# Optimization experiments

Measured on AMD Instinct MI355X. Metric: run time of the kernel, lower is better.

## Reference

```python
import jax, jax.numpy as jnp
import numpy as np

B, S, D, H = 2, 2048, 1024, 16
HW = D // H  # head width = 64
MASK_FILL = -100000000.0


def setup_inputs() -> dict:
    key0 = jax.random.key(0)
    ks = jax.random.split(key0, 12)
    inp = {
        "query": jax.random.normal(ks[0], (B, S, D), jnp.float32),
        "key": jax.random.normal(ks[1], (B, S, D), jnp.float32),
        "value": jax.random.normal(ks[2], (B, S, D), jnp.float32),
        # bool mask, True masks; broadcasts over batch and heads
        "mask": jax.random.randint(ks[3], (S, S), 0, 2).astype(jnp.bool_),
        # per-head projection kernels: (heads, head_width, d_in)
        "Wq": jax.random.normal(ks[4], (H, HW, D), jnp.float32) * 0.02,
        "bq": jnp.zeros((H, HW), jnp.float32),
        "Wk": jax.random.normal(ks[5], (H, HW, D), jnp.float32) * 0.02,
        "bk": jnp.zeros((H, HW), jnp.float32),
        "Wv": jax.random.normal(ks[6], (H, HW, D), jnp.float32) * 0.02,
        "bv": jnp.zeros((H, HW), jnp.float32),
        # collapse projector: contracts (heads, head_width) -> d_output
        "Wo": jax.random.normal(ks[7], (D, H, HW), jnp.float32) * 0.02,
        "bo": jnp.zeros((D,), jnp.float32),
    }
    return inp


def reference(query, key, value, mask, Wq, bq, Wk, bk, Wv, bv, Wo, bo):
    # head projections -> (b, h, s, w)
    q = jnp.einsum("bsd,hwd->bhsw", query, Wq) + bq[:, None, :]
    k = jnp.einsum("btd,hwd->bhtw", key, Wk) + bk[:, None, :]
    v = jnp.einsum("btd,hwd->bhtw", value, Wv) + bv[:, None, :]
    # unscaled logits, masked_fill, softmax (matches original exactly)
    logits = jnp.einsum("bhsw,bhtw->bhst", q, k)
    logits = jnp.where(mask, MASK_FILL, logits)
    score = jax.nn.softmax(logits, axis=-1)
    # NOTE: original divides AV output by sqrt(head_width) AFTER softmax
    attn = jnp.einsum("bhst,bhtw->bhsw", score, v) / jnp.sqrt(jnp.float32(HW))
    # collapse heads -> (b, s, d_output)
    out = jnp.einsum("bhsw,ohw->bso", attn, Wo) + bo
    return out
```

## Files before the change

kernel.cpp:

```cpp
#include <hip/hip_runtime.h>
#include <hip/hip_bf16.h>
#include <math.h>

#define S_LEN   2048
#define D_MODEL 1024
#define N_HEADS 16
#define HEAD_W  64
#define BATCH   2
#define MROWS   (BATCH * S_LEN)
#define MASK_FILL -100000000.0f
#define LOG2E 1.4426950408889634f

typedef __attribute__((ext_vector_type(8))) short bf16x8;
typedef __attribute__((ext_vector_type(4))) float f32x4;
typedef unsigned short u16;
typedef unsigned int   u32;
typedef unsigned long long u64;

__device__ __forceinline__ u16 f2bf(float f) {
    u32 u = __float_as_uint(f);
    return (u16)((u + 0x7fffu + ((u >> 16) & 1u)) >> 16);
}

__device__ __forceinline__ u32 pack_bf16x2(float lo, float hi) {
    __hip_bfloat162 t = __float22bfloat162_rn(make_float2(lo, hi));
    u32 r;
    __builtin_memcpy(&r, &t, 4);
    return r;
}

__device__ __forceinline__ void gld_lds16(const void* gp, void* lp) {
    __builtin_amdgcn_global_load_lds(
        (const __attribute__((address_space(1))) u32*)gp,
        (__attribute__((address_space(3))) u32*)lp, 16, 0, 0);
}

struct CvtJobs {
    const float* src[7];
    u16* dst[7];
    int n[7];
};
__global__ __launch_bounds__(256) void prep_kernel(
    CvtJobs j, const unsigned char* __restrict__ mask, u64* __restrict__ bits) {
    const int t = blockIdx.y;
    if (t < 7) {
        const float* s = j.src[t];
        u16* d = j.dst[t];
        const int n = j.n[t];
        int i = (blockIdx.x * 256 + threadIdx.x) * 4;
        if (i < n) {
            float4 v = *(const float4*)(s + i);
            ushort4 o;
            o.x = f2bf(v.x); o.y = f2bf(v.y); o.z = f2bf(v.z); o.w = f2bf(v.w);
            *(ushort4*)(d + i) = o;
        }
        return;
    }
    if (blockIdx.x >= 2048) return;
    __shared__ int isByte;
    if (threadIdx.x == 0) isByte = 0;
    __syncthreads();
    const int e0 = blockIdx.x * 2048;
    const uint2 v = ((const uint2*)(mask + e0))[threadIdx.x];
    if (((v.x | v.y) & 0xFFFFFF00u) != 0u) isByte = 1;
    __syncthreads();
    const int ib = isByte;
    const int* mi = (const int*)mask;
#pragma unroll
    for (int jj = 0; jj < 8; ++jj) {
        const int e = e0 + jj * 256 + threadIdx.x;
        const bool m = ib ? (mask[e] != 0) : (mi[e] != 0);
        const u64 bl = __ballot(m);
        if ((e & 63) == 0) bits[e >> 6] = bl;
    }
}

__device__ __forceinline__ void gemm_core_64(const u16* __restrict__ A,
                                             const u16* __restrict__ Bt,
                                             int m0, int n0, f32x4 acc[2][4]) {
    __shared__ u16 As[2][2048];
    __shared__ u16 Bs[2][4096];
    const int tid = threadIdx.x;
    const int wv = tid >> 6, ln = tid & 63;
    const int lane16 = ln & 15, quad = ln >> 4;
    const int wr = (wv >> 1) * 32, wc = (wv & 1) * 64;
    const u16* Ap = A + (size_t)(m0 + ln) * D_MODEL + wv * 8;
    const u16* B0 = Bt + (size_t)(n0 + ln) * D_MODEL + wv * 8;
    const u16* B1 = Bt + (size_t)(n0 + 64 + ln) * D_MODEL + wv * 8;

    gld_lds16(Ap, &As[0][wv * 512]);
    gld_lds16(B0, &Bs[0][wv * 1024]);
    gld_lds16(B1, &Bs[0][wv * 1024 + 512]);

    for (int kt = 0; kt < D_MODEL / 32; ++kt) {
        const int buf = kt & 1;
        __syncthreads();
        if (kt < D_MODEL / 32 - 1) {
            const int ko = (kt + 1) * 32;
            gld_lds16(Ap + ko, &As[buf ^ 1][wv * 512]);
            gld_lds16(B0 + ko, &Bs[buf ^ 1][wv * 1024]);
            gld_lds16(B1 + ko, &Bs[buf ^ 1][wv * 1024 + 512]);
        }
        bf16x8 af[2], bfv[4];
#pragma unroll
        for (int mt = 0; mt < 2; ++mt)
            af[mt] = *(const bf16x8*)&As[buf][quad * 512 + (wr + mt * 16 + lane16) * 8];
#pragma unroll
        for (int nt = 0; nt < 4; ++nt)
            bfv[nt] = *(const bf16x8*)&Bs[buf][quad * 1024 + (wc + nt * 16 + lane16) * 8];
#pragma unroll
        for (int mt = 0; mt < 2; ++mt)
#pragma unroll
            for (int nt = 0; nt < 4; ++nt)
                acc[mt][nt] = __builtin_amdgcn_mfma_f32_16x16x32_bf16(
                    af[mt], bfv[nt], acc[mt][nt], 0, 0, 0);
    }
}

__global__ __launch_bounds__(256, 4) void qkv_gemm_kernel(
    const u16* __restrict__ xq, const u16* __restrict__ xk, const u16* __restrict__ xv,
    const u16* __restrict__ wq, const u16* __restrict__ wk, const u16* __restrict__ wv,
    const float* __restrict__ bq, const float* __restrict__ bk, const float* __restrict__ bv,
    u16* __restrict__ qb, u16* __restrict__ kb, u16* __restrict__ vbt) {
    const int z = blockIdx.z;
    const int tid = threadIdx.x;
    const int wvi = tid >> 6, ln = tid & 63;
    const int lane16 = ln & 15, quad = ln >> 4;
    const int wr = (wvi >> 1) * 32, wc = (wvi & 1) * 64;
    f32x4 acc[2][4] = {};

    if (z == 2) {
        const int m0 = (blockIdx.y & 15) * 64;
        const int n0 = (((blockIdx.y >> 4) * 8) + blockIdx.x) * 128;
        gemm_core_64(wv, xv, m0, n0, acc);
#pragma unroll
        for (int mt = 0; mt < 2; ++mt)
#pragma unroll
            for (int r = 0; r < 4; ++r) {
                const int m = m0 + wr + mt * 16 + quad * 4 + r;
                const int h = m >> 6, w = m & 63;
                const float bb = bv[m];
#pragma unroll
                for (int nt = 0; nt < 4; ++nt) {
                    const int n = n0 + wc + nt * 16 + lane16;
                    const int bidx = n >> 11, t = n & 2047;
                    vbt[((size_t)((bidx * N_HEADS + h) * HEAD_W + w)) * S_LEN + t] =
                        f2bf(acc[mt][nt][r] + bb);
                }
            }
        return;
    }

    const u16* A = (z == 0) ? xq : xk;
    const u16* Bt = (z == 0) ? wq : wk;
    const float* bias = (z == 0) ? bq : bk;
    u16* outp = (z == 0) ? qb : kb;
    const float scale = (z == 0) ? LOG2E : 1.0f;
    const int m0 = blockIdx.y * 64, n0 = blockIdx.x * 128;
    gemm_core_64(A, Bt, m0, n0, acc);
#pragma unroll
    for (int nt = 0; nt < 4; ++nt) {
        const int n = n0 + wc + nt * 16 + lane16;
        const float bb = bias[n];
        const int h = n >> 6, w = n & 63;
#pragma unroll
        for (int mt = 0; mt < 2; ++mt)
#pragma unroll
            for (int r = 0; r < 4; ++r) {
                const int m = m0 + wr + mt * 16 + quad * 4 + r;
                const int bidx = m >> 11, s = m & 2047;
                outp[((size_t)((bidx * N_HEADS + h) * S_LEN + s)) * HEAD_W + w] =
                    f2bf((acc[mt][nt][r] + bb) * scale);
            }
    }
}

__global__ __launch_bounds__(256, 4) void out_gemm_kernel(
    const u16* __restrict__ ab, const u16* __restrict__ wo,
    const float* __restrict__ bo, float* __restrict__ out) {
    f32x4 acc[2][4] = {};
    const int m0 = blockIdx.y * 64, n0 = blockIdx.x * 128;
    gemm_core_64(ab, wo, m0, n0, acc);
    const int tid = threadIdx.x;
    const int wvi = tid >> 6, ln = tid & 63;
    const int lane16 = ln & 15, quad = ln >> 4;
    const int wr = (wvi >> 1) * 32, wc = (wvi & 1) * 64;
#pragma unroll
    for (int nt = 0; nt < 4; ++nt) {
        const int n = n0 + wc + nt * 16 + lane16;
        const float bb = bo[n];
#pragma unroll
        for (int mt = 0; mt < 2; ++mt)
#pragma unroll
            for (int r = 0; r < 4; ++r) {
                const int m = m0 + wr + mt * 16 + quad * 4 + r;
                out[(size_t)m * D_MODEL + n] = acc[mt][nt][r] + bb;
            }
    }
}

__global__ __launch_bounds__(256, 3) void attn_kernel(
    const u16* __restrict__ qbuf, const u16* __restrict__ kbuf,
    const u16* __restrict__ vbt, const u64* __restrict__ mbits,
    float* __restrict__ Opart, float* __restrict__ lpart) {
    __shared__ u16 Ks[2][4096];
    __shared__ u16 Vt[2][4096];
    __shared__ u16 Ps[4][32 * 72];
    const int tid = threadIdx.x;
    const int wv = tid >> 6, ln = tid & 63;
    const int lane16 = ln & 15, quad = ln >> 4;
    const int s_blk = blockIdx.x * 128;
    const int h = blockIdx.y;
    const int b = blockIdx.z >> 1, hf = blockIdx.z & 1;
    const int c0 = hf * 16;
    const size_t hb = ((size_t)(b * N_HEADS + h)) * S_LEN * HEAD_W;
    const u16* Qg = qbuf + hb;
    const u16* Kg = kbuf + hb;
    const u16* Vg = vbt + hb;

    bf16x8 qa[2][2];
#pragma unroll
    for (int mt = 0; mt < 2; ++mt)
#pragma unroll
        for (int kk = 0; kk < 2; ++kk)
            qa[mt][kk] = *(const bf16x8*)(Qg +
                (size_t)(s_blk + wv * 32 + mt * 16 + lane16) * HEAD_W + kk * 32 + quad * 8);

    const size_t mrow0 = (size_t)(s_blk + wv * 32 + lane16) * 32;
    const size_t mrow1 = (size_t)(s_blk + wv * 32 + 16 + lane16) * 32;
    u64 mwCur0 = mbits[mrow0 + c0], mwCur1 = mbits[mrow1 + c0];
    u64 mwNx0 = 0, mwNx1 = 0;

    {
        const int t0g = c0 * 64;
        const int i0 = 2 * wv, i1 = 2 * wv + 1;
        gld_lds16(Kg + (size_t)(t0g + ln) * HEAD_W + i0 * 8, &Ks[0][i0 * 512]);
        gld_lds16(Kg + (size_t)(t0g + ln) * HEAD_W + i1 * 8, &Ks[0][i1 * 512]);
        gld_lds16(Vg + (size_t)ln * S_LEN + t0g + i0 * 8, &Vt[0][i0 * 512]);
        gld_lds16(Vg + (size_t)ln * S_LEN + t0g + i1 * 8, &Vt[0][i1 * 512]);
    }

    f32x4 oacc[2][4] = {};
    float lsum[2] = {0.0f, 0.0f};

    for (int ci = 0; ci < 16; ++ci) {
        const int c = c0 + ci;
        const int buf = ci & 1;
        __syncthreads();
        if (ci < 15) {
            const int t1 = (c + 1) * 64;
            const int i0 = 2 * wv, i1 = 2 * wv + 1;
            gld_lds16(Kg + (size_t)(t1 + ln) * HEAD_W + i0 * 8, &Ks[buf ^ 1][i0 * 512]);
            gld_lds16(Kg + (size_t)(t1 + ln) * HEAD_W + i1 * 8, &Ks[buf ^ 1][i1 * 512]);
            gld_lds16(Vg + (size_t)ln * S_LEN + t1 + i0 * 8, &Vt[buf ^ 1][i0 * 512]);
            gld_lds16(Vg + (size_t)ln * S_LEN + t1 + i1 * 8, &Vt[buf ^ 1][i1 * 512]);
            mwNx0 = mbits[mrow0 + c + 1];
            mwNx1 = mbits[mrow1 + c + 1];
        }

        f32x4 st[4][2] = {};
#pragma unroll
        for (int kk = 0; kk < 2; ++kk)
#pragma unroll
            for (int ntT = 0; ntT < 4; ++ntT) {
                bf16x8 kf = *(const bf16x8*)&Ks[buf][(kk * 4 + quad) * 512 + (ntT * 16 + lane16) * 8];
#pragma unroll
                for (int mt = 0; mt < 2; ++mt)
                    st[ntT][mt] = __builtin_amdgcn_mfma_f32_16x16x32_bf16(
                        kf, qa[mt][kk], st[ntT][mt], 0, 0, 0);
            }

#pragma unroll
        for (int mt = 0; mt < 2; ++mt) {
            const u64 mw = mt ? mwCur1 : mwCur0;
            float ls0 = 0.0f, ls1 = 0.0f;
#pragma unroll
            for (int ntT = 0; ntT < 4; ++ntT) {
                const u32 nib = (u32)(mw >> (ntT * 16 + quad * 4)) & 15u;
                float p0 = exp2f(st[ntT][mt][0]); if (nib & 1u) p0 = 0.0f;
                float p1 = exp2f(st[ntT][mt][1]); if (nib & 2u) p1 = 0.0f;
                float p2 = exp2f(st[ntT][mt][2]); if (nib & 4u) p2 = 0.0f;
                float p3 = exp2f(st[ntT][mt][3]); if (nib & 8u) p3 = 0.0f;
                ls0 += p0 + p1;
                ls1 += p2 + p3;
                uint2 pk;
                pk.x = pack_bf16x2(p0, p1);
                pk.y = pack_bf16x2(p2, p3);
                *(uint2*)&Ps[wv][(mt * 16 + lane16) * 72 + ntT * 16 + quad * 4] = pk;
            }
            lsum[mt] += ls0 + ls1;
        }

        bf16x8 pf[2][2];
#pragma unroll
        for (int mt = 0; mt < 2; ++mt)
#pragma unroll
            for (int kk = 0; kk < 2; ++kk)
                pf[mt][kk] = *(const bf16x8*)&Ps[wv][(mt * 16 + lane16) * 72 + kk * 32 + quad * 8];
#pragma unroll
        for (int kk = 0; kk < 2; ++kk)
#pragma unroll
            for (int ntw = 0; ntw < 4; ++ntw) {
                bf16x8 vf = *(const bf16x8*)&Vt[buf][(kk * 4 + quad) * 512 + (ntw * 16 + lane16) * 8];
#pragma unroll
                for (int mt = 0; mt < 2; ++mt)
                    oacc[mt][ntw] = __builtin_amdgcn_mfma_f32_16x16x32_bf16(
                        pf[mt][kk], vf, oacc[mt][ntw], 0, 0, 0);
            }
        mwCur0 = mwNx0; mwCur1 = mwNx1;
    }

    float* OpB = Opart + ((size_t)(hf * 4096 + b * 2048)) * 1024;
#pragma unroll
    for (int mt = 0; mt < 2; ++mt) {
#pragma unroll
        for (int r = 0; r < 4; ++r) {
            const int s = s_blk + wv * 32 + mt * 16 + quad * 4 + r;
            float* dst = OpB + (size_t)s * 1024 + h * 64;
#pragma unroll
            for (int ntw = 0; ntw < 4; ++ntw)
                dst[ntw * 16 + lane16] = oacc[mt][ntw][r];
        }
        float lm = lsum[mt];
        lm += __shfl_xor(lm, 16);
        lm += __shfl_xor(lm, 32);
        if (quad == 0) {
            const int srow = s_blk + wv * 32 + mt * 16 + lane16;
            lpart[(size_t)(hf * 4096 + b * 2048 + srow) * 16 + h] = lm;
        }
    }
}

__global__ __launch_bounds__(256) void combine_kernel(
    const float* __restrict__ Op, const float* __restrict__ lp,
    u16* __restrict__ ab) {
    const int idx4 = blockIdx.x * 256 + threadIdx.x;
    const int row = idx4 >> 8;
    const int d = (idx4 & 255) * 4;
    const int h = d >> 6;
    const float l = lp[(size_t)row * 16 + h] + lp[(size_t)(4096 + row) * 16 + h];
    const float inv = 0.125f / l;
    float4 a = *(const float4*)(Op + (size_t)row * 1024 + d);
    float4 b = *(const float4*)(Op + (size_t)(4096 + row) * 1024 + d);
    ushort4 o;
    o.x = f2bf((a.x + b.x) * inv);
    o.y = f2bf((a.y + b.y) * inv);
    o.z = f2bf((a.z + b.z) * inv);
    o.w = f2bf((a.w + b.w) * inv);
    *(ushort4*)(ab + (size_t)row * 1024 + d) = o;
}

extern "C" void kernel_launch(void* const* d_in, const int* in_sizes, int n_in,
                              void* d_out, int out_size, void* d_ws, size_t ws_size,
                              hipStream_t stream) {
    const float* query = (const float*)d_in[0];
    const float* key   = (const float*)d_in[1];
    const float* value = (const float*)d_in[2];
    const void*  mask  = d_in[3];
    const float* Wq = (const float*)d_in[4];
    const float* bq = (const float*)d_in[5];
    const float* Wk = (const float*)d_in[6];
    const float* bk = (const float*)d_in[7];
    const float* Wv = (const float*)d_in[8];
    const float* bv = (const float*)d_in[9];
    const float* Wo = (const float*)d_in[10];
    const float* bo = (const float*)d_in[11];
    float* out = (float*)d_out;

    char* ws = (char*)d_ws;
    const size_t MB = 1024 * 1024;
    u64* bits = (u64*)ws;
    u16* wob  = (u16*)(ws + 1 * MB);
    u16* qb   = (u16*)(ws + 3 * MB);
    u16* kb   = (u16*)(ws + 11 * MB);
    u16* vbt  = (u16*)(ws + 19 * MB);
    char* uA = ws + 27 * MB;
    u16* xq   = (u16*)(uA);
    u16* xk   = (u16*)(uA + 8 * MB);
    u16* xv   = (u16*)(uA + 16 * MB);
    u16* wqb  = (u16*)(uA + 24 * MB);
    u16* wkb  = (u16*)(uA + 26 * MB);
    u16* wvb  = (u16*)(uA + 28 * MB);
    float* Opart = (float*)(uA);
    float* lpart = (float*)(uA + 32 * MB);
    u16* ab = qb;

    const size_t NACT = (size_t)MROWS * D_MODEL;
    const size_t NW   = (size_t)D_MODEL * D_MODEL;

    CvtJobs j;
    j.src[0] = query; j.dst[0] = xq;  j.n[0] = (int)NACT;
    j.src[1] = key;   j.dst[1] = xk;  j.n[1] = (int)NACT;
    j.src[2] = value; j.dst[2] = xv;  j.n[2] = (int)NACT;
    j.src[3] = Wq;    j.dst[3] = wqb; j.n[3] = (int)NW;
    j.src[4] = Wk;    j.dst[4] = wkb; j.n[4] = (int)NW;
    j.src[5] = Wv;    j.dst[5] = wvb; j.n[5] = (int)NW;
    j.src[6] = Wo;    j.dst[6] = wob; j.n[6] = (int)NW;
    prep_kernel<<<dim3(NACT / 1024, 8), 256, 0, stream>>>(
        j, (const unsigned char*)mask, bits);

    qkv_gemm_kernel<<<dim3(D_MODEL / 128, MROWS / 64, 3), 256, 0, stream>>>(
        xq, xk, xv, wqb, wkb, wvb, bq, bk, bv, qb, kb, vbt);
    attn_kernel<<<dim3(S_LEN / 128, N_HEADS, BATCH * 2), 256, 0, stream>>>(
        qb, kb, vbt, bits, Opart, lpart);
    combine_kernel<<<4096, 256, 0, stream>>>(Opart, lpart, ab);
    out_gemm_kernel<<<dim3(D_MODEL / 128, MROWS / 64), 256, 0, stream>>>(
        ab, wob, bo, out);
}
```

Before: 326.2 us.

## Fuse split-KV combine into output GEMM and enlarge GEMM tiles to 128x128

Removes the separate combine kernel: the output projection GEMM now reads the two fp32 partial attention outputs and partial row sums directly, normalizes and converts them to bf16 in registers, and stores them to LDS as its A operand. The QKV and output GEMMs move from 64x128 to 128x128 tiles with 4x4 MFMA accumulators per wave. LDS double buffering is dropped in favour of single buffers with two barriers per k-step. This saves one kernel launch and a bf16 intermediate round trip, and gives more data reuse per tile. The cost is more register pressure, fewer blocks, and less load/compute overlap now that the GEMM loop is no longer double-buffered.

```diff
diff --git a/kernel.cpp b/kernel.cpp
--- a/kernel.cpp
+++ b/kernel.cpp
@@ -75,41 +75,37 @@
     }
 }
 
-__device__ __forceinline__ void gemm_core_64(const u16* __restrict__ A,
-                                             const u16* __restrict__ Bt,
-                                             int m0, int n0, f32x4 acc[2][4]) {
-    __shared__ u16 As[2][2048];
-    __shared__ u16 Bs[2][4096];
+__device__ __forceinline__ void gemm_core_bf16(const u16* __restrict__ A,
+                                               const u16* __restrict__ Bt,
+                                               int m0, int n0, f32x4 acc[4][4]) {
+    __shared__ u16 As[4096];
+    __shared__ u16 Bs[4096];
     const int tid = threadIdx.x;
     const int wv = tid >> 6, ln = tid & 63;
     const int lane16 = ln & 15, quad = ln >> 4;
-    const int wr = (wv >> 1) * 32, wc = (wv & 1) * 64;
-    const u16* Ap = A + (size_t)(m0 + ln) * D_MODEL + wv * 8;
+    const int wr = (wv >> 1) * 64, wc = (wv & 1) * 64;
+    const u16* A0 = A + (size_t)(m0 + ln) * D_MODEL + wv * 8;
+    const u16* A1 = A0 + (size_t)64 * D_MODEL;
     const u16* B0 = Bt + (size_t)(n0 + ln) * D_MODEL + wv * 8;
-    const u16* B1 = Bt + (size_t)(n0 + 64 + ln) * D_MODEL + wv * 8;
-
-    gld_lds16(Ap, &As[0][wv * 512]);
-    gld_lds16(B0, &Bs[0][wv * 1024]);
-    gld_lds16(B1, &Bs[0][wv * 1024 + 512]);
+    const u16* B1 = B0 + (size_t)64 * D_MODEL;
 
     for (int kt = 0; kt < D_MODEL / 32; ++kt) {
-        const int buf = kt & 1;
+        const int ko = kt * 32;
         __syncthreads();
-        if (kt < D_MODEL / 32 - 1) {
-            const int ko = (kt + 1) * 32;
-            gld_lds16(Ap + ko, &As[buf ^ 1][wv * 512]);
-            gld_lds16(B0 + ko, &Bs[buf ^ 1][wv * 1024]);
-            gld_lds16(B1 + ko, &Bs[buf ^ 1][wv * 1024 + 512]);
-        }
-        bf16x8 af[2], bfv[4];
-#pragma unroll
-        for (int mt = 0; mt < 2; ++mt)
-            af[mt] = *(const bf16x8*)&As[buf][quad * 512 + (wr + mt * 16 + lane16) * 8];
+        gld_lds16(A0 + ko, &As[wv * 1024]);
+        gld_lds16(A1 + ko, &As[wv * 1024 + 512]);
+        gld_lds16(B0 + ko, &Bs[wv * 1024]);
+        gld_lds16(B1 + ko, &Bs[wv * 1024 + 512]);
+        __syncthreads();
+        bf16x8 af[4], bfv[4];
+#pragma unroll
+        for (int mt = 0; mt < 4; ++mt)
+            af[mt] = *(const bf16x8*)&As[quad * 1024 + (wr + mt * 16 + lane16) * 8];
 #pragma unroll
         for (int nt = 0; nt < 4; ++nt)
-            bfv[nt] = *(const bf16x8*)&Bs[buf][quad * 1024 + (wc + nt * 16 + lane16) * 8];
-#pragma unroll
-        for (int mt = 0; mt < 2; ++mt)
+            bfv[nt] = *(const bf16x8*)&Bs[quad * 1024 + (wc + nt * 16 + lane16) * 8];
+#pragma unroll
+        for (int mt = 0; mt < 4; ++mt)
 #pragma unroll
             for (int nt = 0; nt < 4; ++nt)
                 acc[mt][nt] = __builtin_amdgcn_mfma_f32_16x16x32_bf16(
@@ -126,15 +122,15 @@
     const int tid = threadIdx.x;
     const int wvi = tid >> 6, ln = tid & 63;
     const int lane16 = ln & 15, quad = ln >> 4;
-    const int wr = (wvi >> 1) * 32, wc = (wvi & 1) * 64;
-    f32x4 acc[2][4] = {};
+    const int wr = (wvi >> 1) * 64, wc = (wvi & 1) * 64;
+    f32x4 acc[4][4] = {};
 
     if (z == 2) {
-        const int m0 = (blockIdx.y & 15) * 64;
-        const int n0 = (((blockIdx.y >> 4) * 8) + blockIdx.x) * 128;
-        gemm_core_64(wv, xv, m0, n0, acc);
-#pragma unroll
-        for (int mt = 0; mt < 2; ++mt)
+        const int m0 = blockIdx.x * 128;
+        const int n0 = blockIdx.y * 128;
+        gemm_core_bf16(wv, xv, m0, n0, acc);
+#pragma unroll
+        for (int mt = 0; mt < 4; ++mt)
 #pragma unroll
             for (int r = 0; r < 4; ++r) {
                 const int m = m0 + wr + mt * 16 + quad * 4 + r;
@@ -156,15 +152,15 @@
     const float* bias = (z == 0) ? bq : bk;
     u16* outp = (z == 0) ? qb : kb;
     const float scale = (z == 0) ? LOG2E : 1.0f;
-    const int m0 = blockIdx.y * 64, n0 = blockIdx.x * 128;
-    gemm_core_64(A, Bt, m0, n0, acc);
+    const int m0 = blockIdx.y * 128, n0 = blockIdx.x * 128;
+    gemm_core_bf16(A, Bt, m0, n0, acc);
 #pragma unroll
     for (int nt = 0; nt < 4; ++nt) {
         const int n = n0 + wc + nt * 16 + lane16;
         const float bb = bias[n];
         const int h = n >> 6, w = n & 63;
 #pragma unroll
-        for (int mt = 0; mt < 2; ++mt)
+        for (int mt = 0; mt < 4; ++mt)
 #pragma unroll
             for (int r = 0; r < 4; ++r) {
                 const int m = m0 + wr + mt * 16 + quad * 4 + r;
@@ -175,22 +171,99 @@
     }
 }
 
-__global__ __launch_bounds__(256, 4) void out_gemm_kernel(
-    const u16* __restrict__ ab, const u16* __restrict__ wo,
-    const float* __restrict__ bo, float* __restrict__ out) {
-    f32x4 acc[2][4] = {};
-    const int m0 = blockIdx.y * 64, n0 = blockIdx.x * 128;
-    gemm_core_64(ab, wo, m0, n0, acc);
+__global__ __launch_bounds__(256) void outc_kernel(
+    const float* __restrict__ Op, const float* __restrict__ lp,
+    const u16* __restrict__ wo, const float* __restrict__ bo,
+    float* __restrict__ out) {
+    __shared__ u16 As[4096];
+    __shared__ u16 Bs[4096];
     const int tid = threadIdx.x;
-    const int wvi = tid >> 6, ln = tid & 63;
+    const int wv = tid >> 6, ln = tid & 63;
     const int lane16 = ln & 15, quad = ln >> 4;
-    const int wr = (wvi >> 1) * 32, wc = (wvi & 1) * 64;
+    const int wr = (wv >> 1) * 64, wc = (wv & 1) * 64;
+    const int m0 = blockIdx.y * 128, n0 = blockIdx.x * 128;
+    const int r0 = m0 + ln, r1 = m0 + 64 + ln;
+    const u16* B0 = wo + (size_t)(n0 + ln) * D_MODEL + wv * 8;
+    const u16* B1 = B0 + (size_t)64 * D_MODEL;
+    const float* A0a = Op + (size_t)r0 * D_MODEL + wv * 8;
+    const float* A0b = A0a + (size_t)MROWS * D_MODEL;
+    const float* A1a = Op + (size_t)r1 * D_MODEL + wv * 8;
+    const float* A1b = A1a + (size_t)MROWS * D_MODEL;
+
+    f32x4 acc[4][4] = {};
+    float4 a0a[2], a0b[2], a1a[2], a1b[2];
+    float l0a, l0b, l1a, l1b;
+    {
+        const int h = (wv * 8) >> 6;
+#pragma unroll
+        for (int q2 = 0; q2 < 2; ++q2) {
+            a0a[q2] = *(const float4*)(A0a + q2 * 4);
+            a0b[q2] = *(const float4*)(A0b + q2 * 4);
+            a1a[q2] = *(const float4*)(A1a + q2 * 4);
+            a1b[q2] = *(const float4*)(A1b + q2 * 4);
+        }
+        l0a = lp[(size_t)r0 * 16 + h]; l0b = lp[(size_t)(MROWS + r0) * 16 + h];
+        l1a = lp[(size_t)r1 * 16 + h]; l1b = lp[(size_t)(MROWS + r1) * 16 + h];
+    }
+
+    for (int kt = 0; kt < D_MODEL / 32; ++kt) {
+        const int ko = kt * 32;
+        __syncthreads();
+        {
+            const float inv0 = 0.125f * __builtin_amdgcn_rcpf(l0a + l0b);
+            const float inv1 = 0.125f * __builtin_amdgcn_rcpf(l1a + l1b);
+            u32 w0[4], w1[4];
+#pragma unroll
+            for (int q2 = 0; q2 < 2; ++q2) {
+                w0[q2 * 2 + 0] = pack_bf16x2((a0a[q2].x + a0b[q2].x) * inv0,
+                                             (a0a[q2].y + a0b[q2].y) * inv0);
+                w0[q2 * 2 + 1] = pack_bf16x2((a0a[q2].z + a0b[q2].z) * inv0,
+                                             (a0a[q2].w + a0b[q2].w) * inv0);
+                w1[q2 * 2 + 0] = pack_bf16x2((a1a[q2].x + a1b[q2].x) * inv1,
+                                             (a1a[q2].y + a1b[q2].y) * inv1);
+                w1[q2 * 2 + 1] = pack_bf16x2((a1a[q2].z + a1b[q2].z) * inv1,
+                                             (a1a[q2].w + a1b[q2].w) * inv1);
+            }
+            *(uint4*)&As[wv * 1024 + ln * 8]       = *(uint4*)w0;
+            *(uint4*)&As[wv * 1024 + 512 + ln * 8] = *(uint4*)w1;
+        }
+        gld_lds16(B0 + ko, &Bs[wv * 1024]);
+        gld_lds16(B1 + ko, &Bs[wv * 1024 + 512]);
+        if (kt < D_MODEL / 32 - 1) {
+            const int ko1 = ko + 32;
+            const int h = (ko1 + wv * 8) >> 6;
+#pragma unroll
+            for (int q2 = 0; q2 < 2; ++q2) {
+                a0a[q2] = *(const float4*)(A0a + ko1 + q2 * 4);
+                a0b[q2] = *(const float4*)(A0b + ko1 + q2 * 4);
+                a1a[q2] = *(const float4*)(A1a + ko1 + q2 * 4);
+                a1b[q2] = *(const float4*)(A1b + ko1 + q2 * 4);
+            }
+            l0a = lp[(size_t)r0 * 16 + h]; l0b = lp[(size_t)(MROWS + r0) * 16 + h];
+            l1a = lp[(size_t)r1 * 16 + h]; l1b = lp[(size_t)(MROWS + r1) * 16 + h];
+        }
+        __syncthreads();
+        bf16x8 af[4], bfv[4];
+#pragma unroll
+        for (int mt = 0; mt < 4; ++mt)
+            af[mt] = *(const bf16x8*)&As[quad * 1024 + (wr + mt * 16 + lane16) * 8];
+#pragma unroll
+        for (int nt = 0; nt < 4; ++nt)
+            bfv[nt] = *(const bf16x8*)&Bs[quad * 1024 + (wc + nt * 16 + lane16) * 8];
+#pragma unroll
+        for (int mt = 0; mt < 4; ++mt)
+#pragma unroll
+            for (int nt = 0; nt < 4; ++nt)
+                acc[mt][nt] = __builtin_amdgcn_mfma_f32_16x16x32_bf16(
+                    af[mt], bfv[nt], acc[mt][nt], 0, 0, 0);
+    }
+
 #pragma unroll
     for (int nt = 0; nt < 4; ++nt) {
         const int n = n0 + wc + nt * 16 + lane16;
         const float bb = bo[n];
 #pragma unroll
-        for (int mt = 0; mt < 2; ++mt)
+        for (int mt = 0; mt < 4; ++mt)
 #pragma unroll
             for (int r = 0; r < 4; ++r) {
                 const int m = m0 + wr + mt * 16 + quad * 4 + r;
@@ -310,7 +383,7 @@
         mwCur0 = mwNx0; mwCur1 = mwNx1;
     }
 
-    float* OpB = Opart + ((size_t)(hf * 4096 + b * 2048)) * 1024;
+    float* OpB = Opart + ((size_t)(hf * MROWS + b * 2048)) * 1024;
 #pragma unroll
     for (int mt = 0; mt < 2; ++mt) {
 #pragma unroll
@@ -326,28 +399,9 @@
         lm += __shfl_xor(lm, 32);
         if (quad == 0) {
             const int srow = s_blk + wv * 32 + mt * 16 + lane16;
-            lpart[(size_t)(hf * 4096 + b * 2048 + srow) * 16 + h] = lm;
-        }
-    }
-}
-
-__global__ __launch_bounds__(256) void combine_kernel(
-    const float* __restrict__ Op, const float* __restrict__ lp,
-    u16* __restrict__ ab) {
-    const int idx4 = blockIdx.x * 256 + threadIdx.x;
-    const int row = idx4 >> 8;
-    const int d = (idx4 & 255) * 4;
-    const int h = d >> 6;
-    const float l = lp[(size_t)row * 16 + h] + lp[(size_t)(4096 + row) * 16 + h];
-    const float inv = 0.125f / l;
-    float4 a = *(const float4*)(Op + (size_t)row * 1024 + d);
-    float4 b = *(const float4*)(Op + (size_t)(4096 + row) * 1024 + d);
-    ushort4 o;
-    o.x = f2bf((a.x + b.x) * inv);
-    o.y = f2bf((a.y + b.y) * inv);
-    o.z = f2bf((a.z + b.z) * inv);
-    o.w = f2bf((a.w + b.w) * inv);
-    *(ushort4*)(ab + (size_t)row * 1024 + d) = o;
+            lpart[(size_t)(hf * MROWS + b * 2048 + srow) * 16 + h] = lm;
+        }
+    }
 }
 
 extern "C" void kernel_launch(void* const* d_in, const int* in_sizes, int n_in,
@@ -383,7 +437,6 @@
     u16* wvb  = (u16*)(uA + 28 * MB);
     float* Opart = (float*)(uA);
     float* lpart = (float*)(uA + 32 * MB);
-    u16* ab = qb;
 
     const size_t NACT = (size_t)MROWS * D_MODEL;
     const size_t NW   = (size_t)D_MODEL * D_MODEL;
@@ -399,11 +452,10 @@
     prep_kernel<<<dim3(NACT / 1024, 8), 256, 0, stream>>>(
         j, (const unsigned char*)mask, bits);
 
-    qkv_gemm_kernel<<<dim3(D_MODEL / 128, MROWS / 64, 3), 256, 0, stream>>>(
+    qkv_gemm_kernel<<<dim3(D_MODEL / 128, MROWS / 128, 3), 256, 0, stream>>>(
         xq, xk, xv, wqb, wkb, wvb, bq, bk, bv, qb, kb, vbt);
     attn_kernel<<<dim3(S_LEN / 128, N_HEADS, BATCH * 2), 256, 0, stream>>>(
         qb, kb, vbt, bits, Opart, lpart);
-    combine_kernel<<<4096, 256, 0, stream>>>(Opart, lpart, ab);
-    out_gemm_kernel<<<dim3(D_MODEL / 128, MROWS / 64), 256, 0, stream>>>(
-        ab, wob, bo, out);
-}
+    outc_kernel<<<dim3(D_MODEL / 128, MROWS / 128), 256, 0, stream>>>(
+        Opart, lpart, wob, bo, out);
+}
```

After: 349.4 us. 1.07x slower.
